# Optimization experiments

Measured on AMD Instinct MI355X. Metric: run time of the kernel, lower is better.

The kernel has to match this reference:

```python
import jax, jax.numpy as jnp
import numpy as np

# --- hyperparameters (match module defaults) ---
W_CLASSIFY = 1.1          # weight_factor_classify
W_SAMPLE = 1.0            # weight_factor_sample (mid weight add)
LOSS_WEIGHTS = (1.0, 1.0, 1.0)
PARAMS_HEAD = dict(a=80.0, b=1500.0, c=1750.0, d=2000.0, t=-0.5)
PARAMS_CHEST = dict(a=10.0, b=75.0, c=85.0, d=100.0, t=-0.5)
PARAMS_NECK = dict(a=0.15, b=1.5, c=1.7, d=1.9, t=-0.5)

# AIS thresholds (reimplemented in-kernel; original used numpy round-trips)
HEAD_THR = np.array([150.0, 500.0, 1000.0, 1800.0, 2600.0], dtype=np.float32)
CHEST_THR = np.array([22.0, 35.0, 45.0, 55.0, 65.0], dtype=np.float32)
CHEST_OT_SCALE = np.array([0.8, 0.9, 1.0, 1.1, 1.2], dtype=np.float32)  # per occupant-type
NECK_THR = np.array([0.2, 0.5, 1.0, 1.5, 2.0], dtype=np.float32)


def piecewise_linear(y_true, y_pred, p, mid):
    a, b, c, d, t = p['a'], p['b'], p['c'], p['d'], p['t']
    k = -np.log(t + 1.0) / d  # decay rate for y > d
    w = jnp.zeros_like(y_true)
    w = jnp.where((y_true >= 0) & (y_true < a), (mid / a) * y_true, w)
    w = jnp.where((y_true >= a) & (y_true <= b), mid, w)
    w = jnp.where((y_true > b) & (y_true < c), mid - (mid / (c - b)) * (y_true - b), w)
    w = jnp.where((y_true >= c) & (y_true <= d), 0.0, w)
    w = jnp.where(y_true > d, -1.0 + jnp.exp(-k * (y_true - d)), w)
    w = w + jnp.where(y_pred < 0, mid, 0.0)
    return w


def ais_from_thresholds(x, thr):
    # piecewise-constant AIS class: number of thresholds exceeded, in [0, 5]
    return jnp.sum(x[:, None] >= thr[None, :], axis=-1).astype(jnp.float32)


def task_loss(pred, true, ais_pred, ais_true, params):
    # AIS values are classification results of detached values in the
    # original (no grad) -> stop_gradient here.
    w_cls = W_CLASSIFY ** jnp.abs(jax.lax.stop_gradient(ais_pred) - jax.lax.stop_gradient(ais_true))
    w_mid = 1.0 + piecewise_linear(true, pred, params, W_SAMPLE)
    base = jnp.abs(pred - true)  # MAE, reduction='none'
    return jnp.mean(base * w_cls * w_mid)


def setup_inputs() -> dict:
    key = jax.random.key(0)
    k1, k2, k3 = jax.random.split(key, 3)
    B = 4194304
    scales = jnp.array([2500.0, 120.0, 2.5], dtype=jnp.float32)  # HIC, Dmax, Nij ranges
    pred = (jax.random.uniform(k1, (B, 3), dtype=jnp.float32) * 1.1 - 0.05) * scales
    true = jax.random.uniform(k2, (B, 3), dtype=jnp.float32) * scales
    ot = jax.random.randint(k3, (B,), 0, 5, dtype=jnp.int32)
    return {"pred": pred, "true": true, "ot": ot}


def reference(pred, true, ot):
    thr_head = jnp.asarray(HEAD_THR)
    thr_neck = jnp.asarray(NECK_THR)
    # chest thresholds scale with occupant type -> per-sample thresholds
    thr_chest = jnp.asarray(CHEST_THR)[None, :] * jnp.asarray(CHEST_OT_SCALE)[ot][:, None]

    p_hic, p_dmax, p_nij = pred[:, 0], pred[:, 1], pred[:, 2]
    t_hic, t_dmax, t_nij = true[:, 0], true[:, 1], true[:, 2]

    loss_hic = task_loss(p_hic, t_hic,
                         ais_from_thresholds(p_hic, thr_head),
                         ais_from_thresholds(t_hic, thr_head), PARAMS_HEAD)

    ais_p_chest = jnp.sum(p_dmax[:, None] >= thr_chest, axis=-1).astype(jnp.float32)
    ais_t_chest = jnp.sum(t_dmax[:, None] >= thr_chest, axis=-1).astype(jnp.float32)
    loss_dmax = task_loss(p_dmax, t_dmax, ais_p_chest, ais_t_chest, PARAMS_CHEST)

    loss_nij = task_loss(p_nij, t_nij,
                         ais_from_thresholds(p_nij, thr_neck),
                         ais_from_thresholds(t_nij, thr_neck), PARAMS_NECK)

    w_hic, w_dmax, w_nij = LOSS_WEIGHTS
    return w_hic * loss_hic + w_dmax * loss_dmax + w_nij * loss_nij
```

## Files before the change

### kernel.cpp

```cpp
#include <hip/hip_runtime.h>

#define NT 256
#define NB 4096


__device__ __forceinline__ float loss_head(float p, float t) {
    int ap = (p>=150.0f)+(p>=500.0f)+(p>=1000.0f)+(p>=1800.0f)+(p>=2600.0f);
    int at = (t>=150.0f)+(t>=500.0f)+(t>=1000.0f)+(t>=1800.0f)+(t>=2600.0f);
    float wc = exp2f(fabsf((float)(ap-at)) * 0.13750352374993502f);
    float wm = fmaxf(fminf(fminf(t*0.0125f, 1.0f), fmaf(t,-0.004f,7.0f)), 0.0f);
    float tail = exp2f(fmaf(t,-0.0005f,1.0f)) - 1.0f;
    wm = (t>2000.0f) ? tail : wm;
    wm += (p<0.0f) ? 2.0f : 1.0f;
    return fabsf(p-t)*wc*wm;
}

__device__ __forceinline__ float loss_chest(float p, float t, float rs) {
    float ps = p*rs, ts = t*rs;
    int ap = (ps>=22.0f)+(ps>=35.0f)+(ps>=45.0f)+(ps>=55.0f)+(ps>=65.0f);
    int at = (ts>=22.0f)+(ts>=35.0f)+(ts>=45.0f)+(ts>=55.0f)+(ts>=65.0f);
    float wc = exp2f(fabsf((float)(ap-at)) * 0.13750352374993502f);
    float wm = fmaxf(fminf(fminf(t*0.1f, 1.0f), fmaf(t,-0.1f,8.5f)), 0.0f);
    float tail = exp2f(fmaf(t,-0.01f,1.0f)) - 1.0f;
    wm = (t>100.0f) ? tail : wm;
    wm += (p<0.0f) ? 2.0f : 1.0f;
    return fabsf(p-t)*wc*wm;
}

__device__ __forceinline__ float loss_neck(float p, float t) {
    int ap = (p>=0.2f)+(p>=0.5f)+(p>=1.0f)+(p>=1.5f)+(p>=2.0f);
    int at = (t>=0.2f)+(t>=0.5f)+(t>=1.0f)+(t>=1.5f)+(t>=2.0f);
    float wc = exp2f(fabsf((float)(ap-at)) * 0.13750352374993502f);
    float wm = fmaxf(fminf(fminf(t*6.6666667f, 1.0f), fmaf(t,-5.0f,8.5f)), 0.0f);
    float tail = exp2f(fmaf(t,-0.52631579f,1.0f)) - 1.0f;
    wm = (t>1.9f) ? tail : wm;
    wm += (p<0.0f) ? 2.0f : 1.0f;
    return fabsf(p-t)*wc*wm;
}

__device__ __forceinline__ float quad_loss(float4 p0, float4 p1, float4 p2,
                                           float4 t0, float4 t1, float4 t2,
                                           int4 o) {
    float r0 = __builtin_amdgcn_rcpf(fmaf(0.1f,(float)o.x,0.8f));
    float r1 = __builtin_amdgcn_rcpf(fmaf(0.1f,(float)o.y,0.8f));
    float r2 = __builtin_amdgcn_rcpf(fmaf(0.1f,(float)o.z,0.8f));
    float r3 = __builtin_amdgcn_rcpf(fmaf(0.1f,(float)o.w,0.8f));
    float a;
    a  = loss_head (p0.x,t0.x) + loss_chest(p0.y,t0.y,r0) + loss_neck(p0.z,t0.z);
    a += loss_head (p0.w,t0.w) + loss_chest(p1.x,t1.x,r1) + loss_neck(p1.y,t1.y);
    a += loss_head (p1.z,t1.z) + loss_chest(p1.w,t1.w,r2) + loss_neck(p2.x,t2.x);
    a += loss_head (p2.y,t2.y) + loss_chest(p2.z,t2.z,r3) + loss_neck(p2.w,t2.w);
    return a;
}

__global__ __launch_bounds__(NT)
void weighted_loss_main(const float* __restrict__ pred,
                        const float* __restrict__ truth,
                        const int*   __restrict__ ot,
                        float* __restrict__ partial, int B) {
    const int nquad = B >> 2;
    const int g = blockIdx.x * NT + threadIdx.x;
    const int T = gridDim.x * NT;
    const float4* p4 = (const float4*)pred;
    const float4* t4 = (const float4*)truth;
    const int4*   o4 = (const int4*)ot;

    float acc = 0.0f;

    if (g < nquad) {
        for (int q = g; q < nquad; q += T) {
            float4 p0=p4[3*q], p1=p4[3*q+1], p2=p4[3*q+2];
            float4 t0=t4[3*q], t1=t4[3*q+1], t2=t4[3*q+2];
            int4 o = o4[q];
            acc += quad_loss(p0,p1,p2, t0,t1,t2, o);
        }
    }
    for (int r = ((nquad)<<2) + g; r < B; r += T) {
        float rs = __builtin_amdgcn_rcpf(fmaf(0.1f,(float)ot[r],0.8f));
        acc += loss_head (pred[3*r],   truth[3*r])
             + loss_chest(pred[3*r+1], truth[3*r+1], rs)
             + loss_neck (pred[3*r+2], truth[3*r+2]);
    }

    #pragma unroll
    for (int off = 32; off > 0; off >>= 1) acc += __shfl_down(acc, off, 64);
    __shared__ float sm[NT / 64];
    const int lane = threadIdx.x & 63, wid = threadIdx.x >> 6;
    if (lane == 0) sm[wid] = acc;
    __syncthreads();
    if (threadIdx.x == 0) {
        float s = 0.0f;
        #pragma unroll
        for (int w = 0; w < NT / 64; ++w) s += sm[w];
        partial[blockIdx.x] = s;
    }
}

__global__ __launch_bounds__(1024)
void weighted_loss_reduce(const float* __restrict__ partial, int n,
                          float* __restrict__ out, float invB) {
    float acc = 0.0f;
    for (int i = threadIdx.x; i < n; i += blockDim.x) acc += partial[i];
    #pragma unroll
    for (int off = 32; off > 0; off >>= 1) acc += __shfl_down(acc, off, 64);
    __shared__ float sm[16];
    const int lane = threadIdx.x & 63, wid = threadIdx.x >> 6;
    if (lane == 0) sm[wid] = acc;
    __syncthreads();
    if (threadIdx.x == 0) {
        float s = 0.0f;
        #pragma unroll
        for (int w = 0; w < 16; ++w) s += sm[w];
        out[0] = s * invB;
    }
}

extern "C" void kernel_launch(void* const* d_in, const int* in_sizes, int n_in,
                              void* d_out, int out_size, void* d_ws, size_t ws_size,
                              hipStream_t stream) {
    const float* pred  = (const float*)d_in[0];
    const float* truth = (const float*)d_in[1];
    const int*   ot    = (const int*)d_in[2];
    const int B = in_sizes[2];
    float* partial = (float*)d_ws;

    weighted_loss_main<<<NB, NT, 0, stream>>>(pred, truth, ot, partial, B);
    weighted_loss_reduce<<<1, 1024, 0, stream>>>(partial, NB, (float*)d_out,
                                                 1.0f / (float)B);
}
```

Measured before the change: 139.4 us.

## Shrink grid and software-pipeline quad loads across fixed unrolled iterations

Cuts the grid from 4096 to 1024 blocks. When the problem size matches the grid exactly, each thread runs a fully unrolled loop of four iterations that loads the next quad's pred/true/ot vectors while computing the current one. It also adds an occupancy hint to launch bounds. The aim is to overlap memory latency with compute and cut per-block overhead, at the cost of more registers and a specialized path tied to the input size.

```diff
diff --git a/kernel.cpp b/kernel.cpp
--- a/kernel.cpp
+++ b/kernel.cpp
@@ -1,7 +1,8 @@
 #include <hip/hip_runtime.h>
 
 #define NT 256
-#define NB 4096
+#define NB 1024
+#define ITERS 4
 
 
 __device__ __forceinline__ float loss_head(float p, float t) {
@@ -53,7 +54,7 @@
     return a;
 }
 
-__global__ __launch_bounds__(NT)
+__global__ __launch_bounds__(NT, 4)
 void weighted_loss_main(const float* __restrict__ pred,
                         const float* __restrict__ truth,
                         const int*   __restrict__ ot,
@@ -67,19 +68,43 @@
 
     float acc = 0.0f;
 
-    if (g < nquad) {
+    if (nquad == T * ITERS) {
+        float4 P0, P1, P2, Q0, Q1, Q2;  int4 O;
+        {
+            const int q = g;
+            P0 = p4[3*q]; P1 = p4[3*q+1]; P2 = p4[3*q+2];
+            Q0 = t4[3*q]; Q1 = t4[3*q+1]; Q2 = t4[3*q+2];
+            O  = o4[q];
+        }
+        #pragma unroll
+        for (int k = 0; k < ITERS; ++k) {
+            float4 nP0, nP1, nP2, nQ0, nQ1, nQ2;  int4 nO;
+            if (k + 1 < ITERS) {
+                const int q = g + (k + 1) * T;
+                nP0 = p4[3*q]; nP1 = p4[3*q+1]; nP2 = p4[3*q+2];
+                nQ0 = t4[3*q]; nQ1 = t4[3*q+1]; nQ2 = t4[3*q+2];
+                nO  = o4[q];
+            }
+            acc += quad_loss(P0, P1, P2, Q0, Q1, Q2, O);
+            if (k + 1 < ITERS) {
+                P0 = nP0; P1 = nP1; P2 = nP2;
+                Q0 = nQ0; Q1 = nQ1; Q2 = nQ2;
+                O  = nO;
+            }
+        }
+    } else {
         for (int q = g; q < nquad; q += T) {
             float4 p0=p4[3*q], p1=p4[3*q+1], p2=p4[3*q+2];
             float4 t0=t4[3*q], t1=t4[3*q+1], t2=t4[3*q+2];
             int4 o = o4[q];
             acc += quad_loss(p0,p1,p2, t0,t1,t2, o);
         }
-    }
-    for (int r = ((nquad)<<2) + g; r < B; r += T) {
-        float rs = __builtin_amdgcn_rcpf(fmaf(0.1f,(float)ot[r],0.8f));
-        acc += loss_head (pred[3*r],   truth[3*r])
-             + loss_chest(pred[3*r+1], truth[3*r+1], rs)
-             + loss_neck (pred[3*r+2], truth[3*r+2]);
+        for (int r = (nquad<<2) + g; r < B; r += T) {
+            float rs = __builtin_amdgcn_rcpf(fmaf(0.1f,(float)ot[r],0.8f));
+            acc += loss_head (pred[3*r],   truth[3*r])
+                 + loss_chest(pred[3*r+1], truth[3*r+1], rs)
+                 + loss_neck (pred[3*r+2], truth[3*r+2]);
+        }
     }
 
     #pragma unroll
```

Measured after the change: 142.7 us. 2.4% more time.
